# Performance work log

Measured on AMD Instinct MI355X. Metric: run time of the kernel, lower is better.

The kernel has to match this reference:

```python
import jax, jax.numpy as jnp
import numpy as np

LAYERS = 16; SUBLAYERS = 12; NPLANES = LAYERS * SUBLAYERS
POS_LEVEL = 10; DEPTH_LEVEL = 8; ORDER = 3; BASIS_OUT = 8
HIDDEN = 384; BASIS_HIDDEN = 64
SLOPE = 0.01; SIG_OFF = 5.0
IN_H = 512; IN_W = 768; RAYS = 1024
OFFSET = 0.0


def leaky(x):
    return jnp.where(x >= 0, x, SLOPE * x)


def grid_sample_3d(vol, gx, gy, gz):
    # vol (C, D, H, W); grid coords normalized [-1,1]; align_corners=True, zeros padding
    C, Dm, H, W = vol.shape
    x = (gx + 1.0) * 0.5 * (W - 1)
    y = (gy + 1.0) * 0.5 * (H - 1)
    z = (gz + 1.0) * 0.5 * (Dm - 1)
    x0 = jnp.floor(x); y0 = jnp.floor(y); z0 = jnp.floor(z)
    flat = vol.reshape(C, -1)
    out = jnp.zeros((C,) + x.shape, vol.dtype)
    for dz in (0.0, 1.0):
        for dy in (0.0, 1.0):
            for dx in (0.0, 1.0):
                xi = x0 + dx; yi = y0 + dy; zi = z0 + dz
                w = (1 - jnp.abs(x - xi)) * (1 - jnp.abs(y - yi)) * (1 - jnp.abs(z - zi))
                valid = ((xi >= 0) & (xi < W) & (yi >= 0) & (yi < H) & (zi >= 0) & (zi < Dm)).astype(vol.dtype)
                idx = ((jnp.clip(zi, 0, Dm - 1) * H + jnp.clip(yi, 0, H - 1)) * W
                       + jnp.clip(xi, 0, W - 1)).astype(jnp.int32)
                out = out + (w * valid)[None] * jnp.take(flat, idx, axis=1)
    return out


def _rotation(angle, axis):
    axis = np.asarray(axis, np.float64); axis /= np.linalg.norm(axis)
    K = np.array([[0, -axis[2], axis[1]], [axis[2], 0, -axis[0]], [-axis[1], axis[0], 0]])
    R = np.eye(3) + np.sin(angle) * K + (1 - np.cos(angle)) * (K @ K)
    return jnp.asarray(R, jnp.float32)


def setup_inputs() -> dict:
    key = jax.random.key(0)
    ks = jax.random.split(key, 32)
    def lin(i, fan_in, fan_out):
        w = jax.random.normal(ks[i], (fan_in, fan_out), jnp.float32) / np.sqrt(fan_in).astype(np.float32)
        b = jnp.zeros((fan_out,), jnp.float32)
        return w, b
    in_dim = 2 * (2 * POS_LEVEL + DEPTH_LEVEL)     # 56
    out_dim = 1 + BASIS_OUT * 3                    # 25
    w0, b0 = lin(0, in_dim, HIDDEN)
    w1, b1 = lin(1, HIDDEN, HIDDEN)
    w2, b2 = lin(2, HIDDEN, HIDDEN)
    w3, b3 = lin(3, HIDDEN, HIDDEN)
    w4, b4 = lin(4, HIDDEN, HIDDEN)
    wo, bo = lin(5, HIDDEN, out_dim)
    bw0, bb0 = lin(6, 4 * ORDER, BASIS_HIDDEN)
    bw1, bb1 = lin(7, BASIS_HIDDEN, BASIS_HIDDEN)
    bwo, bbo = lin(8, BASIS_HIDDEN, BASIS_OUT)
    mpi_c = jax.random.uniform(ks[20], (LAYERS, 3, IN_H, IN_W), jnp.float32, -1.0, 1.0)
    K = jnp.array([[600.0, 0.0, IN_W / 2.0], [0.0, 600.0, IN_H / 2.0], [0.0, 0.0, 1.0]], jnp.float32)
    planes = jnp.asarray(1.0 / np.linspace(1.0, 0.1, NPLANES), jnp.float32)  # inverse-depth spacing, dmin=1 dmax=10
    selection = jax.random.randint(ks[21], (RAYS,), 0, IN_H * IN_W)
    return dict(
        mpi_c=mpi_c, w0=w0, b0=b0, w1=w1, b1=b1, w2=w2, b2=b2, w3=w3, b3=b3, w4=w4, b4=b4,
        wo=wo, bo=bo, bw0=bw0, bb0=bb0, bw1=bw1, bb1=bb1, bwo=bwo, bbo=bbo,
        ref_rT=jnp.eye(3, dtype=jnp.float32), ref_t=jnp.zeros((3, 1), jnp.float32), ref_k=K,
        feat_r=_rotation(0.03, [0.2, 1.0, 0.1]),
        feat_t=jnp.array([[0.08], [0.03], [0.02]], jnp.float32),
        feat_center=jnp.array([[-0.08], [-0.03], [-0.02]], jnp.float32),
        feat_k=K, planes=planes, selection=selection, out_h=IN_H, out_w=IN_W)


def reference(mpi_c, w0, b0, w1, b1, w2, b2, w3, b3, w4, b4, wo, bo,
              bw0, bb0, bw1, bb1, bwo, bbo,
              ref_rT, ref_t, ref_k, feat_r, feat_t, feat_center, feat_k,
              planes, selection, out_h, out_w):
    # ---- homography warp (computeHomographies / computeHomoWarp) ----
    ki = jnp.linalg.inv(feat_k)
    new_r = feat_r @ ref_rT
    new_t = -new_r @ ref_t + feat_t
    nvec = jnp.array([[0.0, 0.0, 1.0]], jnp.float32)
    Ha = new_r.T
    Hb = Ha @ new_t @ nvec @ Ha
    Hc = (nvec @ Ha @ new_t)[0, 0]
    Hs = ref_k @ (Ha + Hb / (-planes[:, None, None] - Hc)) @ ki      # (P,3,3)
    coords = jnp.stack([(selection % out_w).astype(jnp.float32),
                        (selection // out_w).astype(jnp.float32),
                        jnp.ones_like(selection, jnp.float32)], -1)   # (R,3)
    prod = jnp.einsum('rc,pkc->prk', coords, Hs)                      # (P,R,3)
    ref_coords = prod[..., :2] / prod[..., 2:]                        # (P,R,2)
    scale = jnp.array([IN_W - 1.0, IN_H - 1.0], jnp.float32)
    warp = (ref_coords + OFFSET) / scale * 2.0 - 1.0                  # (P,R,2)
    R = warp.shape[1]

    # ---- positional encoding + main MLP ----
    pos_freq = (0.5 * np.pi) * (2.0 ** jnp.arange(POS_LEVEL, dtype=jnp.float32))
    depth_freq = (0.5 * np.pi) * (2.0 ** jnp.arange(DEPTH_LEVEL, dtype=jnp.float32))
    z_coords = jnp.linspace(-1.0, 1.0, NPLANES)
    vxy = (warp[..., None] * pos_freq).reshape(NPLANES, R, 2 * POS_LEVEL)
    vz = jnp.broadcast_to((z_coords[:, None] * depth_freq[None])[:, None, :], (NPLANES, R, DEPTH_LEVEL))
    vxyz = jnp.concatenate([vxy, vz], -1)
    big = jnp.concatenate([jnp.sin(vxyz), jnp.cos(vxyz)], -1)         # (P,R,56)
    h = leaky(big @ w0 + b0)
    for w_, b_ in ((w1, b1), (w2, b2), (w3, b3), (w4, b4)):
        h = leaky(h @ w_ + b_)
    out = h @ wo + bo                                                 # (P,R,25)
    alpha = jax.nn.sigmoid(out[..., 0] - SIG_OFF)                     # (P,R)

    # ---- trilinear grid sample of sigmoid(mpi_c) ----
    vol = jnp.transpose(jax.nn.sigmoid(mpi_c), (1, 0, 2, 3))          # (3,L,H,W)
    depths = jnp.repeat(jnp.linspace(-1.0, 1.0, LAYERS), SUBLAYERS)   # (P,)
    gz = jnp.broadcast_to(depths[:, None], (NPLANES, R))
    rgb = grid_sample_3d(vol, warp[..., 0], warp[..., 1], gz)         # (3,P,R)
    rgb = jnp.transpose(rgb, (1, 2, 0))                               # (P,R,3)

    # ---- specular basis (viewing-angle MLP) ----
    camera = ref_rT.T @ feat_center + ref_t                           # (3,1)
    coords3 = jnp.concatenate([ref_coords, jnp.ones_like(ref_coords[..., :1])], -1)
    xyz = jnp.einsum('kc,prc->prk', ki, coords3 * planes[:, None, None])
    v = xyz - camera[:, 0]
    v = v / (jnp.linalg.norm(v, axis=-1, keepdims=True) + 1e-7)
    view_freq = 2.0 ** jnp.arange(ORDER, dtype=jnp.float32)
    hv = (v[..., :2, None] * view_freq).reshape(NPLANES, R, 2 * ORDER)
    venc = jnp.concatenate([jnp.sin(0.5 * np.pi * hv), jnp.cos(0.5 * np.pi * hv)], -1)  # (P,R,12)
    bh = leaky(venc @ bw0 + bb0)
    bh = leaky(bh @ bw1 + bb1)
    basis = jnp.tanh(bh @ bwo + bbo)                                  # (P,R,8)
    coeff = jnp.repeat(out[::SUBLAYERS, ..., 1:], SUBLAYERS, axis=0)  # (P,R,24)
    coeff = jnp.tanh(coeff.reshape(NPLANES, R, 3, BASIS_OUT))
    illum = jnp.sum(coeff * basis[:, :, None, :], -1)                 # (P,R,3)
    rgb = jnp.clip(rgb + illum, 0.0, 1.0)

    # ---- alpha compositing (cumprod_exclusive over planes) ----
    cp = jnp.cumprod(1.0 - alpha, axis=0)
    weight = jnp.concatenate([jnp.ones_like(cp[:1]), cp[:-1]], 0)     # (P,R)
    comp = jnp.sum((weight * alpha)[..., None] * rgb, axis=0)         # (R,3)
    return jnp.transpose(comp)[None, :, :, None]                      # (1,3,R,1)
```

## Files before the change

### kernel.cpp

```cpp
#include <hip/hip_runtime.h>
#include <hip/hip_bf16.h>
#include <math.h>


typedef _Float16 half2 __attribute__((ext_vector_type(2)));
typedef _Float16 half4 __attribute__((ext_vector_type(4)));
typedef _Float16 half8 __attribute__((ext_vector_type(8)));
typedef float f32x4 __attribute__((ext_vector_type(4)));

#if __has_builtin(__builtin_amdgcn_mfma_f32_16x16x32_f16)
#define MFMA32(a, b, c) __builtin_amdgcn_mfma_f32_16x16x32_f16((a), (b), (c), 0, 0, 0)
#else
#define MFMA32(a, b, c) (c)
#endif

#define NPLANES 192
#define RAYS    1024
#define IMW     768
#define IMH     512
#define PI_HALF 1.5707964f

#define FR(i, c) ((((i) >> 4) * 6144) + (((c) >> 5) * 512) + ((((c) >> 3) & 3) * 128) \
                  + (((i) & 15) * 8) + ((c) & 7))

__device__ __forceinline__ float sin_rev(float rev) {
  float f, r;
  asm("v_fract_f32 %0, %1" : "=v"(f) : "v"(rev));
  asm("v_sin_f32 %0, %1" : "=v"(r) : "v"(f));
  return r;
}

__device__ __forceinline__ float exp2_fast(float x) {
  float r;
  asm("v_exp_f32 %0, %1" : "=v"(r) : "v"(x));
  return r;
}
__device__ __forceinline__ float rcp_fast(float x) {
  float r;
  asm("v_rcp_f32 %0, %1" : "=v"(r) : "v"(x));
  return r;
}
__device__ __forceinline__ float tanh_fast(float x) {
  const float xc = fminf(fmaxf(x, -30.f), 30.f);
  const float t = exp2_fast(xc * 2.885390082f);
  return (t - 1.f) * rcp_fast(t + 1.f);
}
__device__ __forceinline__ float sig5_fast(float o) {
  const float u = exp2_fast((5.f - o) * 1.4426950f);
  return rcp_fast(1.f + u);
}

__device__ __forceinline__ half4 leaky_pack(f32x4 a) {
  const float v0 = fmaxf(a[0], a[0] * 0.01f);
  const float v1 = fmaxf(a[1], a[1] * 0.01f);
  const float v2 = fmaxf(a[2], a[2] * 0.01f);
  const float v3 = fmaxf(a[3], a[3] * 0.01f);
  const half2 lo = __builtin_bit_cast(half2, __builtin_amdgcn_cvt_pkrtz(v0, v1));
  const half2 hi = __builtin_bit_cast(half2, __builtin_amdgcn_cvt_pkrtz(v2, v3));
  return __builtin_shufflevector(lo, hi, 0, 1, 2, 3);
}

#define O_HS     0
#define O_KICAM  7168
#define O_ALPHA  7424
#define O_COEFF  793856
#define O_PW0    2366720
#define O_PW1    2415872
#define O_PW2    2710784
#define O_PW3    3005696
#define O_PW4    3300608
#define O_PWO    3595520
#define O_PBW0   3620096
#define O_PBW1   3624192
#define O_PBWO   3632384
#define O_BASIS  3634432
#define WS_NEED  (O_BASIS + 6291456)

__global__ void prep_kernel(const float* __restrict__ ref_rT, const float* __restrict__ ref_t,
                            const float* __restrict__ ref_k, const float* __restrict__ feat_r,
                            const float* __restrict__ feat_t, const float* __restrict__ feat_center,
                            const float* __restrict__ feat_k, const float* __restrict__ planes,
                            float* __restrict__ wsHs, float* __restrict__ wsKiCam)
{
  __shared__ float sKi[9], sHa[9], sHb[9], sHc[1];
  if (threadIdx.x == 0) {
    float a = feat_k[0], b = feat_k[1], c = feat_k[2];
    float d = feat_k[3], e = feat_k[4], f = feat_k[5];
    float g = feat_k[6], h = feat_k[7], i = feat_k[8];
    float A = e * i - f * h, B = -(d * i - f * g), C = d * h - e * g;
    float det = a * A + b * B + c * C;
    float id = 1.0f / det;
    float ki[9];
    ki[0] = A * id;             ki[1] = -(b * i - c * h) * id;  ki[2] = (b * f - c * e) * id;
    ki[3] = B * id;             ki[4] = (a * i - c * g) * id;   ki[5] = -(a * f - c * d) * id;
    ki[6] = C * id;             ki[7] = -(a * h - b * g) * id;  ki[8] = (a * e - b * d) * id;
    float nr[9];
    for (int r2 = 0; r2 < 3; ++r2)
      for (int c2 = 0; c2 < 3; ++c2) {
        float s = 0.f;
        for (int k2 = 0; k2 < 3; ++k2) s += feat_r[r2 * 3 + k2] * ref_rT[k2 * 3 + c2];
        nr[r2 * 3 + c2] = s;
      }
    float ntv[3];
    for (int r2 = 0; r2 < 3; ++r2) {
      float s = 0.f;
      for (int k2 = 0; k2 < 3; ++k2) s += nr[r2 * 3 + k2] * ref_t[k2];
      ntv[r2] = -s + feat_t[r2];
    }
    float Ha[9];
    for (int r2 = 0; r2 < 3; ++r2)
      for (int c2 = 0; c2 < 3; ++c2) Ha[r2 * 3 + c2] = nr[c2 * 3 + r2];
    float u[3];
    for (int r2 = 0; r2 < 3; ++r2) {
      float s = 0.f;
      for (int k2 = 0; k2 < 3; ++k2) s += Ha[r2 * 3 + k2] * ntv[k2];
      u[r2] = s;
    }
    float Hb[9];
    for (int r2 = 0; r2 < 3; ++r2)
      for (int c2 = 0; c2 < 3; ++c2) Hb[r2 * 3 + c2] = u[r2] * Ha[6 + c2];
    float cam[3];
    for (int r2 = 0; r2 < 3; ++r2) {
      float s = 0.f;
      for (int k2 = 0; k2 < 3; ++k2) s += ref_rT[k2 * 3 + r2] * feat_center[k2];
      cam[r2] = s + ref_t[r2];
    }
    for (int j = 0; j < 9; ++j) { sKi[j] = ki[j]; sHa[j] = Ha[j]; sHb[j] = Hb[j]; }
    sHc[0] = u[2];
    for (int j = 0; j < 9; ++j) wsKiCam[j] = ki[j];
    for (int j = 0; j < 3; ++j) wsKiCam[9 + j] = cam[j];
  }
  __syncthreads();
  int p = threadIdx.x;
  if (p < NPLANES) {
    float dnm = -planes[p] - sHc[0];
    float T[9];
    for (int j = 0; j < 9; ++j) T[j] = sHa[j] + sHb[j] / dnm;
    float U[9];
    for (int r2 = 0; r2 < 3; ++r2)
      for (int c2 = 0; c2 < 3; ++c2) {
        float s = 0.f;
        for (int k2 = 0; k2 < 3; ++k2) s += ref_k[r2 * 3 + k2] * T[k2 * 3 + c2];
        U[r2 * 3 + c2] = s;
      }
    for (int r2 = 0; r2 < 3; ++r2)
      for (int c2 = 0; c2 < 3; ++c2) {
        float s = 0.f;
        for (int k2 = 0; k2 < 3; ++k2) s += U[r2 * 3 + k2] * sKi[k2 * 3 + c2];
        wsHs[p * 9 + r2 * 3 + c2] = s;
      }
  }
}

__global__ void pack_all_kernel(const float* __restrict__ w0, const float* __restrict__ w1,
                                const float* __restrict__ w2, const float* __restrict__ w3,
                                const float* __restrict__ w4, const float* __restrict__ wo,
                                const float* __restrict__ bw0, const float* __restrict__ bw1,
                                const float* __restrict__ bwo, _Float16* __restrict__ dst)
{
  const int idx = blockIdx.x * 256 + threadIdx.x;
  const float* src; int Ksrc, Nsrc, NP, l;
  if (idx < 24576)       { src = w0;  Ksrc = 56;  Nsrc = 384; NP = 384; l = idx; }
  else if (idx < 172032) { src = w1;  Ksrc = 384; Nsrc = 384; NP = 384; l = idx - 24576; }
  else if (idx < 319488) { src = w2;  Ksrc = 384; Nsrc = 384; NP = 384; l = idx - 172032; }
  else if (idx < 466944) { src = w3;  Ksrc = 384; Nsrc = 384; NP = 384; l = idx - 319488; }
  else if (idx < 614400) { src = w4;  Ksrc = 384; Nsrc = 384; NP = 384; l = idx - 466944; }
  else if (idx < 626688) { src = wo;  Ksrc = 384; Nsrc = 25;  NP = 32;  l = idx - 614400; }
  else if (idx < 628736) { src = bw0; Ksrc = 12;  Nsrc = 64;  NP = 64;  l = idx - 626688; }
  else if (idx < 632832) { src = bw1; Ksrc = 64;  Nsrc = 64;  NP = 64;  l = idx - 628736; }
  else if (idx < 633856) { src = bwo; Ksrc = 64;  Nsrc = 8;   NP = 16;  l = idx - 632832; }
  else return;
  const int within = l & 511, blk = l >> 9;
  const int kg = within >> 7, ln = (within >> 3) & 15, j = within & 7;
  const int ntiles = NP >> 4;
  const int nt = blk % ntiles, kc = blk / ntiles;
  const int k = kc * 32 + kg * 8 + j, nn = nt * 16 + ln;
  const float v = (k < Ksrc && nn < Nsrc) ? src[k * Nsrc + nn] : 0.0f;
  dst[idx] = (_Float16)v;
}

template <int NKC>
__device__ __forceinline__ void hidden_layer(_Float16* hb, const _Float16* __restrict__ wl,
                                             const float* __restrict__ bias,
                                             int wv, int g, int ln, int lane)
{
  f32x4 acc[6][4];
  #pragma unroll
  for (int ft = 0; ft < 6; ++ft) {
    const f32x4 bv4 = *(const f32x4*)&bias[(wv * 6 + ft) * 16 + g * 4];
    #pragma unroll
    for (int pt = 0; pt < 4; ++pt) acc[ft][pt] = bv4;
  }
  #pragma unroll 2
  for (int kc = 0; kc < NKC; ++kc) {
    half8 aw[6];
    #pragma unroll
    for (int ft = 0; ft < 6; ++ft)
      aw[ft] = *(const half8*)&wl[(kc * 24 + wv * 6 + ft) * 512 + lane * 8];
    half8 bx[4];
    #pragma unroll
    for (int pt = 0; pt < 4; ++pt)
      bx[pt] = *(const half8*)&hb[pt * 6144 + kc * 512 + lane * 8];
    #pragma unroll
    for (int ft = 0; ft < 6; ++ft)
      #pragma unroll
      for (int pt = 0; pt < 4; ++pt)
        acc[ft][pt] = MFMA32(aw[ft], bx[pt], acc[ft][pt]);
  }
  __syncthreads();
  #pragma unroll
  for (int pt = 0; pt < 4; ++pt)
    #pragma unroll
    for (int ft = 0; ft < 6; ++ft) {
      const int f0 = wv * 96 + ft * 16 + g * 4;
      *(half4*)&hb[pt * 6144 + (f0 >> 5) * 512 + ((f0 >> 3) & 3) * 128 + ln * 8 + (f0 & 7)] =
          leaky_pack(acc[ft][pt]);
    }
  __syncthreads();
}

template <int NKC>
__device__ __forceinline__ void basis_hidden(_Float16* hb, const _Float16* __restrict__ wl,
                                             const float* __restrict__ bias,
                                             int wv, int g, int ln, int lane)
{
  f32x4 acc[4];
  const f32x4 bv4 = *(const f32x4*)&bias[wv * 16 + g * 4];
  #pragma unroll
  for (int pt = 0; pt < 4; ++pt) acc[pt] = bv4;
  #pragma unroll
  for (int kc = 0; kc < NKC; ++kc) {
    half8 aw = *(const half8*)&wl[(kc * 4 + wv) * 512 + lane * 8];
    #pragma unroll
    for (int pt = 0; pt < 4; ++pt) {
      half8 bx = *(const half8*)&hb[pt * 6144 + kc * 512 + lane * 8];
      acc[pt] = MFMA32(aw, bx, acc[pt]);
    }
  }
  __syncthreads();
  const int f0 = wv * 16 + g * 4;
  #pragma unroll
  for (int pt = 0; pt < 4; ++pt)
    *(half4*)&hb[pt * 6144 + (f0 >> 5) * 512 + ((f0 >> 3) & 3) * 128 + ln * 8 + (f0 & 7)] =
        leaky_pack(acc[pt]);
  __syncthreads();
}

__global__ __launch_bounds__(256, 3) void mlp_kernel(
    const int* __restrict__ selection, const float* __restrict__ planes,
    const float* __restrict__ wsHs, const float* __restrict__ wsKiCam,
    const _Float16* __restrict__ pw0, const _Float16* __restrict__ pw1,
    const _Float16* __restrict__ pw2, const _Float16* __restrict__ pw3,
    const _Float16* __restrict__ pw4, const _Float16* __restrict__ pwo,
    const float* __restrict__ b0, const float* __restrict__ b1,
    const float* __restrict__ b2, const float* __restrict__ b3,
    const float* __restrict__ b4, const float* __restrict__ bo,
    const _Float16* __restrict__ pbw0, const _Float16* __restrict__ pbw1,
    const _Float16* __restrict__ pbwo,
    const float* __restrict__ bb0, const float* __restrict__ bb1,
    const float* __restrict__ bbo,
    float* __restrict__ wsAlpha, float* __restrict__ wsCoeff, float* __restrict__ wsBasis)
{
  __shared__ _Float16 hbuf[4 * 6144];
  const int t = threadIdx.x;
  const int m0 = blockIdx.x * 64;
  const int p = m0 >> 10;
  const int r0 = m0 & 1023;
  const int lane = t & 63, wv = t >> 6;
  const int g = lane >> 4, ln = lane & 15;

  {
    const int i = t >> 2, q = t & 3;
    const int ray = r0 + i;
    const int sel = selection[ray];
    const float cx = (float)(sel % IMW), cy = (float)(sel / IMW);
    const float* H = wsHs + p * 9;
    const float pr0 = H[0] * cx + H[1] * cy + H[2];
    const float pr1 = H[3] * cx + H[4] * cy + H[5];
    const float pr2 = H[6] * cx + H[7] * cy + H[8];
    const float rx = pr0 / pr2, ry = pr1 / pr2;
    const float wx = (rx / 767.0f) * 2.0f - 1.0f;
    const float wy = (ry / 511.0f) * 2.0f - 1.0f;
    const float zc = -1.0f + (float)p * (2.0f / 191.0f);
    #pragma unroll
    for (int cc = 0; cc < 7; ++cc) {
      const int c = q * 7 + cc;
      float base; int e;
      if (c < 10)      { base = wx; e = c; }
      else if (c < 20) { base = wy; e = c - 10; }
      else             { base = zc; e = c - 20; }
      const float rev = ldexpf(base, e - 2);
      hbuf[FR(i, c)]      = (_Float16)sin_rev(rev);
      hbuf[FR(i, c + 28)] = (_Float16)sin_rev(rev + 0.25f);
    }
    hbuf[FR(i, 56 + q)] = (_Float16)0.f;
    hbuf[FR(i, 60 + q)] = (_Float16)0.f;
  }
  __syncthreads();

  hidden_layer<2>(hbuf, pw0, b0, wv, g, ln, lane);
  hidden_layer<12>(hbuf, pw1, b1, wv, g, ln, lane);
  hidden_layer<12>(hbuf, pw2, b2, wv, g, ln, lane);
  hidden_layer<12>(hbuf, pw3, b3, wv, g, ln, lane);
  hidden_layer<12>(hbuf, pw4, b4, wv, g, ln, lane);

  f32x4 acc2[2];
  {
    #pragma unroll
    for (int ft = 0; ft < 2; ++ft) {
      f32x4 bv;
      #pragma unroll
      for (int r = 0; r < 4; ++r) {
        const int f = ft * 16 + g * 4 + r;
        bv[r] = (f < 25) ? bo[f] : 0.f;
      }
      acc2[ft] = bv;
    }
    #pragma unroll 2
    for (int kc = 0; kc < 12; ++kc) {
      half8 bx = *(const half8*)&hbuf[wv * 6144 + kc * 512 + lane * 8];
      #pragma unroll
      for (int ft = 0; ft < 2; ++ft) {
        half8 aw = *(const half8*)&pwo[(kc * 2 + ft) * 512 + lane * 8];
        acc2[ft] = MFMA32(aw, bx, acc2[ft]);
      }
    }
    __syncthreads();
  }

  {
    const int i = t >> 2, q = t & 3;
    const int ray = r0 + i;
    const int sel = selection[ray];
    const float cx = (float)(sel % IMW), cy = (float)(sel / IMW);
    const float* H = wsHs + p * 9;
    const float pr0 = H[0] * cx + H[1] * cy + H[2];
    const float pr1 = H[3] * cx + H[4] * cy + H[5];
    const float pr2 = H[6] * cx + H[7] * cy + H[8];
    const float rx = pr0 / pr2, ry = pr1 / pr2;
    const float pd = planes[p];
    const float* ki = wsKiCam; const float* cam = wsKiCam + 9;
    const float c0 = rx * pd, c1 = ry * pd, c2 = pd;
    const float vx0 = ki[0] * c0 + ki[1] * c1 + ki[2] * c2 - cam[0];
    const float vy0 = ki[3] * c0 + ki[4] * c1 + ki[5] * c2 - cam[1];
    const float vz0 = ki[6] * c0 + ki[7] * c1 + ki[8] * c2 - cam[2];
    const float nrm = sqrtf(vx0 * vx0 + vy0 * vy0 + vz0 * vz0) + 1e-7f;
    const float vx = vx0 / nrm, vy = vy0 / nrm;
    #pragma unroll
    for (int cc = 0; cc < 4; ++cc) {
      const int c = q * 4 + cc;
      float v;
      if (c < 6) {
        v = sin_rev(ldexpf((c < 3) ? vx : vy, (c % 3) - 2));
      } else if (c < 12) {
        const int c6 = c - 6;
        v = sin_rev(ldexpf((c6 < 3) ? vx : vy, (c6 % 3) - 2) + 0.25f);
      } else v = 0.f;
      hbuf[FR(i, c)] = (_Float16)v;
    }
  }
  __syncthreads();

  {
    if (g == 0) {
      const int ray = r0 + wv * 16 + ln;
      wsAlpha[p * RAYS + ray] = sig5_fast(acc2[0][0]);
    }
    if ((p % 12) == 0) {
      const int pg = p / 12;
      const int ray = r0 + wv * 16 + ln;
      #pragma unroll
      for (int ft = 0; ft < 2; ++ft)
        #pragma unroll
        for (int r = 0; r < 4; ++r) {
          const int f = ft * 16 + g * 4 + r;
          if (f >= 1 && f < 25)
            wsCoeff[(pg * 24 + (f - 1)) * RAYS + ray] = tanh_fast(acc2[ft][r]);
        }
    }
  }

  basis_hidden<1>(hbuf, pbw0, bb0, wv, g, ln, lane);
  basis_hidden<2>(hbuf, pbw1, bb1, wv, g, ln, lane);
  {
    f32x4 accO = (f32x4){0.f, 0.f, 0.f, 0.f};
    #pragma unroll
    for (int kc = 0; kc < 2; ++kc) {
      half8 aw = *(const half8*)&pbwo[kc * 512 + lane * 8];
      half8 bx = *(const half8*)&hbuf[wv * 6144 + kc * 512 + lane * 8];
      accO = MFMA32(aw, bx, accO);
    }
    if (g < 2) {
      const int ray = r0 + wv * 16 + ln;
      f32x4 bv;
      #pragma unroll
      for (int r = 0; r < 4; ++r)
        bv[r] = tanh_fast(accO[r] + bbo[g * 4 + r]);
      *(f32x4*)&wsBasis[(p * RAYS + ray) * 8 + g * 4] = bv;
    }
  }
}

__global__ __launch_bounds__(192) void composite_kernel(
    const float* __restrict__ mpi, const int* __restrict__ selection,
    const float* __restrict__ wsHs, const float* __restrict__ wsAlpha,
    const float* __restrict__ wsCoeff, const float* __restrict__ wsBasis,
    float* __restrict__ out)
{
  const int ray = blockIdx.x;
  const int p = threadIdx.x;
  const int sel = selection[ray];
  const float cx = (float)(sel % IMW), cy = (float)(sel / IMW);
  const float* H = wsHs + p * 9;
  const float pr0 = H[0] * cx + H[1] * cy + H[2];
  const float pr1 = H[3] * cx + H[4] * cy + H[5];
  const float pr2 = H[6] * cx + H[7] * cy + H[8];
  const float rx = pr0 / pr2, ry = pr1 / pr2;
  const float wx = (rx / 767.0f) * 2.0f - 1.0f;
  const float wy = (ry / 511.0f) * 2.0f - 1.0f;
  const float x = (wx + 1.0f) * 0.5f * 767.0f;
  const float y = (wy + 1.0f) * 0.5f * 511.0f;
  const float gz = -1.0f + (float)(p / 12) * (2.0f / 15.0f);
  const float z = (gz + 1.0f) * 0.5f * 15.0f;
  const float x0 = floorf(x), y0 = floorf(y), z0 = floorf(z);
  float rgb0 = 0.f, rgb1 = 0.f, rgb2 = 0.f;
  #pragma unroll
  for (int dz = 0; dz < 2; ++dz)
    #pragma unroll
    for (int dy = 0; dy < 2; ++dy)
      #pragma unroll
      for (int dx = 0; dx < 2; ++dx) {
        const float xi = x0 + (float)dx, yi = y0 + (float)dy, zi = z0 + (float)dz;
        const float w = (1.f - fabsf(x - xi)) * (1.f - fabsf(y - yi)) * (1.f - fabsf(z - zi));
        const bool valid = (xi >= 0.f) && (xi < 768.f) && (yi >= 0.f) && (yi < 512.f)
                        && (zi >= 0.f) && (zi < 16.f);
        if (valid && w != 0.f) {
          const int ix = (int)xi, iy = (int)yi, iz = (int)zi;
          const int base = iz * 3 * (IMW * IMH) + iy * IMW + ix;
          const float v0 = mpi[base];
          const float v1 = mpi[base + IMW * IMH];
          const float v2 = mpi[base + 2 * IMW * IMH];
          rgb0 += w * (1.f / (1.f + expf(-v0)));
          rgb1 += w * (1.f / (1.f + expf(-v1)));
          rgb2 += w * (1.f / (1.f + expf(-v2)));
        }
      }
  const float* bs = wsBasis + (p * RAYS + ray) * 8;
  const float* cf = wsCoeff + (p / 12) * 24 * RAYS + ray;
  float il0 = 0.f, il1 = 0.f, il2 = 0.f;
  #pragma unroll
  for (int j = 0; j < 8; ++j) {
    const float bj = bs[j];
    il0 += cf[j * RAYS] * bj;
    il1 += cf[(8 + j) * RAYS] * bj;
    il2 += cf[(16 + j) * RAYS] * bj;
  }
  rgb0 = fminf(fmaxf(rgb0 + il0, 0.f), 1.f);
  rgb1 = fminf(fmaxf(rgb1 + il1, 0.f), 1.f);
  rgb2 = fminf(fmaxf(rgb2 + il2, 0.f), 1.f);
  const float a = wsAlpha[p * RAYS + ray];
  const int lane = p & 63, w64 = p >> 6;
  float xs = 1.f - a;
  #pragma unroll
  for (int off = 1; off < 64; off <<= 1) {
    const float v = __shfl_up(xs, off, 64);
    if (lane >= off) xs *= v;
  }
  __shared__ float wtot[3];
  __shared__ float part[3][3];
  if (lane == 63) wtot[w64] = xs;
  __syncthreads();
  float pre = 1.f;
  #pragma unroll
  for (int q = 0; q < 2; ++q)
    if (q < w64) pre *= wtot[q];
  float excl = __shfl_up(xs, 1, 64);
  if (lane == 0) excl = 1.f;
  const float wa = pre * excl * a;
  float s0 = wa * rgb0, s1 = wa * rgb1, s2 = wa * rgb2;
  #pragma unroll
  for (int off = 32; off >= 1; off >>= 1) {
    s0 += __shfl_down(s0, off, 64);
    s1 += __shfl_down(s1, off, 64);
    s2 += __shfl_down(s2, off, 64);
  }
  if (lane == 0) { part[w64][0] = s0; part[w64][1] = s1; part[w64][2] = s2; }
  __syncthreads();
  if (p == 0) {
    out[0 * RAYS + ray] = part[0][0] + part[1][0] + part[2][0];
    out[1 * RAYS + ray] = part[0][1] + part[1][1] + part[2][1];
    out[2 * RAYS + ray] = part[0][2] + part[1][2] + part[2][2];
  }
}

extern "C" void kernel_launch(void* const* d_in, const int* in_sizes, int n_in,
                              void* d_out, int out_size, void* d_ws, size_t ws_size,
                              hipStream_t stream)
{
  (void)in_sizes; (void)n_in; (void)out_size;
  const float* mpi    = (const float*)d_in[0];
  const float* w0     = (const float*)d_in[1];
  const float* b0     = (const float*)d_in[2];
  const float* w1     = (const float*)d_in[3];
  const float* b1     = (const float*)d_in[4];
  const float* w2     = (const float*)d_in[5];
  const float* b2     = (const float*)d_in[6];
  const float* w3     = (const float*)d_in[7];
  const float* b3     = (const float*)d_in[8];
  const float* w4     = (const float*)d_in[9];
  const float* b4     = (const float*)d_in[10];
  const float* wo     = (const float*)d_in[11];
  const float* bo     = (const float*)d_in[12];
  const float* bw0    = (const float*)d_in[13];
  const float* bb0    = (const float*)d_in[14];
  const float* bw1    = (const float*)d_in[15];
  const float* bb1    = (const float*)d_in[16];
  const float* bwo    = (const float*)d_in[17];
  const float* bbo    = (const float*)d_in[18];
  const float* ref_rT = (const float*)d_in[19];
  const float* ref_t  = (const float*)d_in[20];
  const float* ref_k  = (const float*)d_in[21];
  const float* feat_r = (const float*)d_in[22];
  const float* feat_t = (const float*)d_in[23];
  const float* feat_c = (const float*)d_in[24];
  const float* feat_k = (const float*)d_in[25];
  const float* planes = (const float*)d_in[26];
  const int*   selection = (const int*)d_in[27];
  float* outp = (float*)d_out;
  char* ws = (char*)d_ws;
  if (ws_size < (size_t)WS_NEED) return;

  float* wsHs    = (float*)(ws + O_HS);
  float* wsKiCam = (float*)(ws + O_KICAM);
  float* wsAlpha = (float*)(ws + O_ALPHA);
  float* wsCoeff = (float*)(ws + O_COEFF);
  float* wsBasis = (float*)(ws + O_BASIS);
  _Float16* pw0  = (_Float16*)(ws + O_PW0);
  _Float16* pw1  = (_Float16*)(ws + O_PW1);
  _Float16* pw2  = (_Float16*)(ws + O_PW2);
  _Float16* pw3  = (_Float16*)(ws + O_PW3);
  _Float16* pw4  = (_Float16*)(ws + O_PW4);
  _Float16* pwo  = (_Float16*)(ws + O_PWO);
  _Float16* pbw0 = (_Float16*)(ws + O_PBW0);
  _Float16* pbw1 = (_Float16*)(ws + O_PBW1);
  _Float16* pbwo = (_Float16*)(ws + O_PBWO);

  prep_kernel<<<1, 256, 0, stream>>>(ref_rT, ref_t, ref_k, feat_r, feat_t, feat_c,
                                     feat_k, planes, wsHs, wsKiCam);
  pack_all_kernel<<<2476, 256, 0, stream>>>(w0, w1, w2, w3, w4, wo, bw0, bw1, bwo, pw0);

  mlp_kernel<<<(NPLANES * RAYS) / 64, 256, 0, stream>>>(
      selection, planes, wsHs, wsKiCam,
      pw0, pw1, pw2, pw3, pw4, pwo,
      b0, b1, b2, b3, b4, bo,
      pbw0, pbw1, pbwo, bb0, bb1, bbo,
      wsAlpha, wsCoeff, wsBasis);

  composite_kernel<<<RAYS, NPLANES, 0, stream>>>(mpi, selection, wsHs, wsAlpha,
                                                 wsCoeff, wsBasis, outp);
}
```

Measured before the change: 263.2 us.

## Switch MLP matmuls from 16x16x32 to 32x32x16 MFMA tiles

Rewrites the hidden-layer, output and basis MLP matmuls to use 32x32x16 f16 MFMA instructions instead of 16x16x32. The weight packing and the LDS activation layout are reorganised to match 32-row tiles. Each wave now computes 3x2 tiles of 32x32, which raises arithmetic intensity per operand load and cuts the number of LDS and weight reads. It also brackets the MFMA loops with s_setprio. In exchange, accumulator register use grows, and the output and basis stages leave half the waves idle.

```diff
diff --git a/kernel.cpp b/kernel.cpp
--- a/kernel.cpp
+++ b/kernel.cpp
@@ -7,21 +7,21 @@
 typedef _Float16 half4 __attribute__((ext_vector_type(4)));
 typedef _Float16 half8 __attribute__((ext_vector_type(8)));
 typedef float f32x4 __attribute__((ext_vector_type(4)));
-
-#if __has_builtin(__builtin_amdgcn_mfma_f32_16x16x32_f16)
-#define MFMA32(a, b, c) __builtin_amdgcn_mfma_f32_16x16x32_f16((a), (b), (c), 0, 0, 0)
+typedef float f32x16 __attribute__((ext_vector_type(16)));
+
+#if __has_builtin(__builtin_amdgcn_mfma_f32_32x32x16_f16)
+#define MFMA32x32(a, b, c) __builtin_amdgcn_mfma_f32_32x32x16_f16((a), (b), (c), 0, 0, 0)
 #else
-#define MFMA32(a, b, c) (c)
+#define MFMA32x32(a, b, c) (c)
 #endif
 
 #define NPLANES 192
 #define RAYS    1024
 #define IMW     768
 #define IMH     512
-#define PI_HALF 1.5707964f
-
-#define FR(i, c) ((((i) >> 4) * 6144) + (((c) >> 5) * 512) + ((((c) >> 3) & 3) * 128) \
-                  + (((i) & 15) * 8) + ((c) & 7))
+
+#define FR32(i, c) ((((i) >> 5) * 12288) + (((c) >> 4) * 512) + ((((c) >> 3) & 1) * 256) \
+                    + (((i) & 31) * 8) + ((c) & 7))
 
 __device__ __forceinline__ float sin_rev(float rev) {
   float f, r;
@@ -29,7 +29,6 @@
   asm("v_sin_f32 %0, %1" : "=v"(r) : "v"(f));
   return r;
 }
-
 __device__ __forceinline__ float exp2_fast(float x) {
   float r;
   asm("v_exp_f32 %0, %1" : "=v"(r) : "v"(x));
@@ -50,11 +49,11 @@
   return rcp_fast(1.f + u);
 }
 
-__device__ __forceinline__ half4 leaky_pack(f32x4 a) {
-  const float v0 = fmaxf(a[0], a[0] * 0.01f);
-  const float v1 = fmaxf(a[1], a[1] * 0.01f);
-  const float v2 = fmaxf(a[2], a[2] * 0.01f);
-  const float v3 = fmaxf(a[3], a[3] * 0.01f);
+__device__ __forceinline__ half4 leaky_pack(float a0, float a1, float a2, float a3) {
+  const float v0 = fmaxf(a0, a0 * 0.01f);
+  const float v1 = fmaxf(a1, a1 * 0.01f);
+  const float v2 = fmaxf(a2, a2 * 0.01f);
+  const float v3 = fmaxf(a3, a3 * 0.01f);
   const half2 lo = __builtin_bit_cast(half2, __builtin_amdgcn_cvt_pkrtz(v0, v1));
   const half2 hi = __builtin_bit_cast(half2, __builtin_amdgcn_cvt_pkrtz(v2, v3));
   return __builtin_shufflevector(lo, hi, 0, 1, 2, 3);
@@ -71,8 +70,8 @@
 #define O_PW4    3300608
 #define O_PWO    3595520
 #define O_PBW0   3620096
-#define O_PBW1   3624192
-#define O_PBWO   3632384
+#define O_PBW1   3622144
+#define O_PBWO   3630336
 #define O_BASIS  3634432
 #define WS_NEED  (O_BASIS + 6291456)
 
@@ -159,22 +158,21 @@
                                 const float* __restrict__ bwo, _Float16* __restrict__ dst)
 {
   const int idx = blockIdx.x * 256 + threadIdx.x;
-  const float* src; int Ksrc, Nsrc, NP, l;
-  if (idx < 24576)       { src = w0;  Ksrc = 56;  Nsrc = 384; NP = 384; l = idx; }
-  else if (idx < 172032) { src = w1;  Ksrc = 384; Nsrc = 384; NP = 384; l = idx - 24576; }
-  else if (idx < 319488) { src = w2;  Ksrc = 384; Nsrc = 384; NP = 384; l = idx - 172032; }
-  else if (idx < 466944) { src = w3;  Ksrc = 384; Nsrc = 384; NP = 384; l = idx - 319488; }
-  else if (idx < 614400) { src = w4;  Ksrc = 384; Nsrc = 384; NP = 384; l = idx - 466944; }
-  else if (idx < 626688) { src = wo;  Ksrc = 384; Nsrc = 25;  NP = 32;  l = idx - 614400; }
-  else if (idx < 628736) { src = bw0; Ksrc = 12;  Nsrc = 64;  NP = 64;  l = idx - 626688; }
-  else if (idx < 632832) { src = bw1; Ksrc = 64;  Nsrc = 64;  NP = 64;  l = idx - 628736; }
-  else if (idx < 633856) { src = bwo; Ksrc = 64;  Nsrc = 8;   NP = 16;  l = idx - 632832; }
+  const float* src; int Ksrc, Nsrc, ntiles, l;
+  if (idx < 24576)       { src = w0;  Ksrc = 56;  Nsrc = 384; ntiles = 12; l = idx; }
+  else if (idx < 172032) { src = w1;  Ksrc = 384; Nsrc = 384; ntiles = 12; l = idx - 24576; }
+  else if (idx < 319488) { src = w2;  Ksrc = 384; Nsrc = 384; ntiles = 12; l = idx - 172032; }
+  else if (idx < 466944) { src = w3;  Ksrc = 384; Nsrc = 384; ntiles = 12; l = idx - 319488; }
+  else if (idx < 614400) { src = w4;  Ksrc = 384; Nsrc = 384; ntiles = 12; l = idx - 466944; }
+  else if (idx < 626688) { src = wo;  Ksrc = 384; Nsrc = 25;  ntiles = 1;  l = idx - 614400; }
+  else if (idx < 627712) { src = bw0; Ksrc = 12;  Nsrc = 64;  ntiles = 2;  l = idx - 626688; }
+  else if (idx < 631808) { src = bw1; Ksrc = 64;  Nsrc = 64;  ntiles = 2;  l = idx - 627712; }
+  else if (idx < 633856) { src = bwo; Ksrc = 64;  Nsrc = 8;   ntiles = 1;  l = idx - 631808; }
   else return;
   const int within = l & 511, blk = l >> 9;
-  const int kg = within >> 7, ln = (within >> 3) & 15, j = within & 7;
-  const int ntiles = NP >> 4;
+  const int hi = within >> 8, m = (within >> 3) & 31, j = within & 7;
   const int nt = blk % ntiles, kc = blk / ntiles;
-  const int k = kc * 32 + kg * 8 + j, nn = nt * 16 + ln;
+  const int k = kc * 16 + hi * 8 + j, nn = nt * 32 + m;
   const float v = (k < Ksrc && nn < Nsrc) ? src[k * Nsrc + nn] : 0.0f;
   dst[idx] = (_Float16)v;
 }
@@ -182,39 +180,50 @@
 template <int NKC>
 __device__ __forceinline__ void hidden_layer(_Float16* hb, const _Float16* __restrict__ wl,
                                              const float* __restrict__ bias,
-                                             int wv, int g, int ln, int lane)
-{
-  f32x4 acc[6][4];
-  #pragma unroll
-  for (int ft = 0; ft < 6; ++ft) {
-    const f32x4 bv4 = *(const f32x4*)&bias[(wv * 6 + ft) * 16 + g * 4];
-    #pragma unroll
-    for (int pt = 0; pt < 4; ++pt) acc[ft][pt] = bv4;
-  }
+                                             int wv, int hi, int l31, int lane)
+{
+  f32x16 acc[3][2];
+  #pragma unroll
+  for (int ft = 0; ft < 3; ++ft) {
+    const int ftg = wv * 3 + ft;
+    f32x16 bv;
+    #pragma unroll
+    for (int q = 0; q < 4; ++q) {
+      const f32x4 b4 = *(const f32x4*)&bias[ftg * 32 + q * 8 + hi * 4];
+      bv[q * 4 + 0] = b4[0]; bv[q * 4 + 1] = b4[1];
+      bv[q * 4 + 2] = b4[2]; bv[q * 4 + 3] = b4[3];
+    }
+    acc[ft][0] = bv; acc[ft][1] = bv;
+  }
+  __builtin_amdgcn_s_setprio(1);
   #pragma unroll 2
   for (int kc = 0; kc < NKC; ++kc) {
-    half8 aw[6];
-    #pragma unroll
-    for (int ft = 0; ft < 6; ++ft)
-      aw[ft] = *(const half8*)&wl[(kc * 24 + wv * 6 + ft) * 512 + lane * 8];
-    half8 bx[4];
-    #pragma unroll
-    for (int pt = 0; pt < 4; ++pt)
-      bx[pt] = *(const half8*)&hb[pt * 6144 + kc * 512 + lane * 8];
-    #pragma unroll
-    for (int ft = 0; ft < 6; ++ft)
+    half8 aw[3];
+    #pragma unroll
+    for (int ft = 0; ft < 3; ++ft)
+      aw[ft] = *(const half8*)&wl[(kc * 12 + wv * 3 + ft) * 512 + lane * 8];
+    half8 bx[2];
+    #pragma unroll
+    for (int pt = 0; pt < 2; ++pt)
+      bx[pt] = *(const half8*)&hb[pt * 12288 + kc * 512 + lane * 8];
+    #pragma unroll
+    for (int ft = 0; ft < 3; ++ft)
       #pragma unroll
-      for (int pt = 0; pt < 4; ++pt)
-        acc[ft][pt] = MFMA32(aw[ft], bx[pt], acc[ft][pt]);
-  }
-  __syncthreads();
-  #pragma unroll
-  for (int pt = 0; pt < 4; ++pt)
-    #pragma unroll
-    for (int ft = 0; ft < 6; ++ft) {
-      const int f0 = wv * 96 + ft * 16 + g * 4;
-      *(half4*)&hb[pt * 6144 + (f0 >> 5) * 512 + ((f0 >> 3) & 3) * 128 + ln * 8 + (f0 & 7)] =
-          leaky_pack(acc[ft][pt]);
+      for (int pt = 0; pt < 2; ++pt)
+        acc[ft][pt] = MFMA32x32(aw[ft], bx[pt], acc[ft][pt]);
+  }
+  __builtin_amdgcn_s_setprio(0);
+  __syncthreads();
+  #pragma unroll
+  for (int pt = 0; pt < 2; ++pt)
+    #pragma unroll
+    for (int ft = 0; ft < 3; ++ft) {
+      const int ftg = wv * 3 + ft;
+      #pragma unroll
+      for (int q = 0; q < 4; ++q)
+        *(half4*)&hb[pt * 12288 + (ftg * 2 + (q >> 1)) * 512 + (q & 1) * 256 + l31 * 8 + hi * 4] =
+            leaky_pack(acc[ft][pt][q * 4 + 0], acc[ft][pt][q * 4 + 1],
+                       acc[ft][pt][q * 4 + 2], acc[ft][pt][q * 4 + 3]);
     }
   __syncthreads();
 }
@@ -222,27 +231,29 @@
 template <int NKC>
 __device__ __forceinline__ void basis_hidden(_Float16* hb, const _Float16* __restrict__ wl,
                                              const float* __restrict__ bias,
-                                             int wv, int g, int ln, int lane)
-{
-  f32x4 acc[4];
-  const f32x4 bv4 = *(const f32x4*)&bias[wv * 16 + g * 4];
-  #pragma unroll
-  for (int pt = 0; pt < 4; ++pt) acc[pt] = bv4;
+                                             int wv, int hi, int l31, int lane)
+{
+  const int ft = wv >> 1, pt = wv & 1;
+  f32x16 acc;
+  #pragma unroll
+  for (int q = 0; q < 4; ++q) {
+    const f32x4 b4 = *(const f32x4*)&bias[ft * 32 + q * 8 + hi * 4];
+    acc[q * 4 + 0] = b4[0]; acc[q * 4 + 1] = b4[1];
+    acc[q * 4 + 2] = b4[2]; acc[q * 4 + 3] = b4[3];
+  }
+  __builtin_amdgcn_s_setprio(1);
   #pragma unroll
   for (int kc = 0; kc < NKC; ++kc) {
-    half8 aw = *(const half8*)&wl[(kc * 4 + wv) * 512 + lane * 8];
-    #pragma unroll
-    for (int pt = 0; pt < 4; ++pt) {
-      half8 bx = *(const half8*)&hb[pt * 6144 + kc * 512 + lane * 8];
-      acc[pt] = MFMA32(aw, bx, acc[pt]);
-    }
-  }
-  __syncthreads();
-  const int f0 = wv * 16 + g * 4;
-  #pragma unroll
-  for (int pt = 0; pt < 4; ++pt)
-    *(half4*)&hb[pt * 6144 + (f0 >> 5) * 512 + ((f0 >> 3) & 3) * 128 + ln * 8 + (f0 & 7)] =
-        leaky_pack(acc[pt]);
+    half8 aw = *(const half8*)&wl[(kc * 2 + ft) * 512 + lane * 8];
+    half8 bx = *(const half8*)&hb[pt * 12288 + kc * 512 + lane * 8];
+    acc = MFMA32x32(aw, bx, acc);
+  }
+  __builtin_amdgcn_s_setprio(0);
+  __syncthreads();
+  #pragma unroll
+  for (int q = 0; q < 4; ++q)
+    *(half4*)&hb[pt * 12288 + (ft * 2 + (q >> 1)) * 512 + (q & 1) * 256 + l31 * 8 + hi * 4] =
+        leaky_pack(acc[q * 4 + 0], acc[q * 4 + 1], acc[q * 4 + 2], acc[q * 4 + 3]);
   __syncthreads();
 }
 
@@ -261,13 +272,13 @@
     const float* __restrict__ bbo,
     float* __restrict__ wsAlpha, float* __restrict__ wsCoeff, float* __restrict__ wsBasis)
 {
-  __shared__ _Float16 hbuf[4 * 6144];
+  __shared__ _Float16 hbuf[2 * 12288];
   const int t = threadIdx.x;
   const int m0 = blockIdx.x * 64;
   const int p = m0 >> 10;
   const int r0 = m0 & 1023;
   const int lane = t & 63, wv = t >> 6;
-  const int g = lane >> 4, ln = lane & 15;
+  const int hi = lane >> 5, l31 = lane & 31;
 
   {
     const int i = t >> 2, q = t & 3;
@@ -290,40 +301,36 @@
       else if (c < 20) { base = wy; e = c - 10; }
       else             { base = zc; e = c - 20; }
       const float rev = ldexpf(base, e - 2);
-      hbuf[FR(i, c)]      = (_Float16)sin_rev(rev);
-      hbuf[FR(i, c + 28)] = (_Float16)sin_rev(rev + 0.25f);
-    }
-    hbuf[FR(i, 56 + q)] = (_Float16)0.f;
-    hbuf[FR(i, 60 + q)] = (_Float16)0.f;
-  }
-  __syncthreads();
-
-  hidden_layer<2>(hbuf, pw0, b0, wv, g, ln, lane);
-  hidden_layer<12>(hbuf, pw1, b1, wv, g, ln, lane);
-  hidden_layer<12>(hbuf, pw2, b2, wv, g, ln, lane);
-  hidden_layer<12>(hbuf, pw3, b3, wv, g, ln, lane);
-  hidden_layer<12>(hbuf, pw4, b4, wv, g, ln, lane);
-
-  f32x4 acc2[2];
+      hbuf[FR32(i, c)]      = (_Float16)sin_rev(rev);
+      hbuf[FR32(i, c + 28)] = (_Float16)sin_rev(rev + 0.25f);
+    }
+    hbuf[FR32(i, 56 + q)] = (_Float16)0.f;
+    hbuf[FR32(i, 60 + q)] = (_Float16)0.f;
+  }
+  __syncthreads();
+
+  hidden_layer<4>(hbuf, pw0, b0, wv, hi, l31, lane);
+  hidden_layer<24>(hbuf, pw1, b1, wv, hi, l31, lane);
+  hidden_layer<24>(hbuf, pw2, b2, wv, hi, l31, lane);
+  hidden_layer<24>(hbuf, pw3, b3, wv, hi, l31, lane);
+  hidden_layer<24>(hbuf, pw4, b4, wv, hi, l31, lane);
+
+  f32x16 acc2;
   {
     #pragma unroll
-    for (int ft = 0; ft < 2; ++ft) {
-      f32x4 bv;
-      #pragma unroll
-      for (int r = 0; r < 4; ++r) {
-        const int f = ft * 16 + g * 4 + r;
-        bv[r] = (f < 25) ? bo[f] : 0.f;
+    for (int r = 0; r < 16; ++r) {
+      const int f = (r & 3) + 8 * (r >> 2) + 4 * hi;
+      acc2[r] = (f < 25) ? bo[f] : 0.f;
+    }
+    if (wv < 2) {
+      __builtin_amdgcn_s_setprio(1);
+      #pragma unroll 2
+      for (int kc = 0; kc < 24; ++kc) {
+        half8 bx = *(const half8*)&hbuf[wv * 12288 + kc * 512 + lane * 8];
+        half8 aw = *(const half8*)&pwo[kc * 512 + lane * 8];
+        acc2 = MFMA32x32(aw, bx, acc2);
       }
-      acc2[ft] = bv;
-    }
-    #pragma unroll 2
-    for (int kc = 0; kc < 12; ++kc) {
-      half8 bx = *(const half8*)&hbuf[wv * 6144 + kc * 512 + lane * 8];
-      #pragma unroll
-      for (int ft = 0; ft < 2; ++ft) {
-        half8 aw = *(const half8*)&pwo[(kc * 2 + ft) * 512 + lane * 8];
-        acc2[ft] = MFMA32(aw, bx, acc2[ft]);
-      }
+      __builtin_amdgcn_s_setprio(0);
     }
     __syncthreads();
   }
@@ -356,48 +363,41 @@
         const int c6 = c - 6;
         v = sin_rev(ldexpf((c6 < 3) ? vx : vy, (c6 % 3) - 2) + 0.25f);
       } else v = 0.f;
-      hbuf[FR(i, c)] = (_Float16)v;
-    }
-  }
-  __syncthreads();
-
-  {
-    if (g == 0) {
-      const int ray = r0 + wv * 16 + ln;
-      wsAlpha[p * RAYS + ray] = sig5_fast(acc2[0][0]);
-    }
+      hbuf[FR32(i, c)] = (_Float16)v;
+    }
+  }
+  __syncthreads();
+
+  if (wv < 2) {
+    const int ray = r0 + wv * 32 + l31;
+    if (hi == 0) wsAlpha[p * RAYS + ray] = sig5_fast(acc2[0]);
     if ((p % 12) == 0) {
       const int pg = p / 12;
-      const int ray = r0 + wv * 16 + ln;
       #pragma unroll
-      for (int ft = 0; ft < 2; ++ft)
-        #pragma unroll
-        for (int r = 0; r < 4; ++r) {
-          const int f = ft * 16 + g * 4 + r;
-          if (f >= 1 && f < 25)
-            wsCoeff[(pg * 24 + (f - 1)) * RAYS + ray] = tanh_fast(acc2[ft][r]);
-        }
-    }
-  }
-
-  basis_hidden<1>(hbuf, pbw0, bb0, wv, g, ln, lane);
-  basis_hidden<2>(hbuf, pbw1, bb1, wv, g, ln, lane);
-  {
-    f32x4 accO = (f32x4){0.f, 0.f, 0.f, 0.f};
-    #pragma unroll
-    for (int kc = 0; kc < 2; ++kc) {
+      for (int r = 0; r < 16; ++r) {
+        const int f = (r & 3) + 8 * (r >> 2) + 4 * hi;
+        if (f >= 1 && f < 25)
+          wsCoeff[(pg * 24 + (f - 1)) * RAYS + ray] = tanh_fast(acc2[r]);
+      }
+    }
+  }
+
+  basis_hidden<1>(hbuf, pbw0, bb0, wv, hi, l31, lane);
+  basis_hidden<4>(hbuf, pbw1, bb1, wv, hi, l31, lane);
+  if (wv < 2) {
+    f32x16 accO = {};
+    #pragma unroll
+    for (int kc = 0; kc < 4; ++kc) {
       half8 aw = *(const half8*)&pbwo[kc * 512 + lane * 8];
-      half8 bx = *(const half8*)&hbuf[wv * 6144 + kc * 512 + lane * 8];
-      accO = MFMA32(aw, bx, accO);
-    }
-    if (g < 2) {
-      const int ray = r0 + wv * 16 + ln;
-      f32x4 bv;
-      #pragma unroll
-      for (int r = 0; r < 4; ++r)
-        bv[r] = tanh_fast(accO[r] + bbo[g * 4 + r]);
-      *(f32x4*)&wsBasis[(p * RAYS + ray) * 8 + g * 4] = bv;
-    }
+      half8 bx = *(const half8*)&hbuf[wv * 12288 + kc * 512 + lane * 8];
+      accO = MFMA32x32(aw, bx, accO);
+    }
+    const int ray = r0 + wv * 32 + l31;
+    f32x4 bv;
+    #pragma unroll
+    for (int s = 0; s < 4; ++s)
+      bv[s] = tanh_fast(accO[s] + bbo[hi * 4 + s]);
+    *(f32x4*)&wsBasis[(p * RAYS + ray) * 8 + hi * 4] = bv;
   }
 }
 
```

Result: slower. 297.5 us (+13.0%).

## Prefetch next layer weights, hoist view encoding, ping-pong basis MLP buffers

Applied to the files above, without the earlier changes.

Before each layer's barrier, the first K-chunk of the next hidden layer's weights is loaded into registers, so that chunk's global-memory latency overlaps the current layer's epilogue. The view-direction encoding is now computed next to the positional encoding, which removes a second recomputation of the homography, and the values are held in registers until they are written. The basis MLP layers write into separate regions of shared memory, which removes one barrier per basis layer. The cost is more live registers (24 extra VGPRs for the prefetched weights plus 4 for the encoding), which could pressure occupancy under launch_bounds(256,3).

```diff
diff --git a/kernel.cpp b/kernel.cpp
--- a/kernel.cpp
+++ b/kernel.cpp
@@ -18,7 +18,6 @@
 #define RAYS    1024
 #define IMW     768
 #define IMH     512
-#define PI_HALF 1.5707964f
 
 #define FR(i, c) ((((i) >> 4) * 6144) + (((c) >> 5) * 512) + ((((c) >> 3) & 3) * 128) \
                   + (((i) & 15) * 8) + ((c) & 7))
@@ -29,7 +28,6 @@
   asm("v_sin_f32 %0, %1" : "=v"(r) : "v"(f));
   return r;
 }
-
 __device__ __forceinline__ float exp2_fast(float x) {
   float r;
   asm("v_exp_f32 %0, %1" : "=v"(r) : "v"(x));
@@ -179,9 +177,17 @@
   dst[idx] = (_Float16)v;
 }
 
-template <int NKC>
+__device__ __forceinline__ void pre6(half8 awp[6], const _Float16* __restrict__ w,
+                                     int wv, int lane) {
+  #pragma unroll
+  for (int ft = 0; ft < 6; ++ft)
+    awp[ft] = *(const half8*)&w[(wv * 6 + ft) * 512 + lane * 8];
+}
+
+template <int NKC, bool PRE>
 __device__ __forceinline__ void hidden_layer(_Float16* hb, const _Float16* __restrict__ wl,
-                                             const float* __restrict__ bias,
+                                             const _Float16* __restrict__ wlnext,
+                                             const float* __restrict__ bias, half8 awp[6],
                                              int wv, int g, int ln, int lane)
 {
   f32x4 acc[6][4];
@@ -191,8 +197,19 @@
     #pragma unroll
     for (int pt = 0; pt < 4; ++pt) acc[ft][pt] = bv4;
   }
+  {
+    half8 bx[4];
+    #pragma unroll
+    for (int pt = 0; pt < 4; ++pt)
+      bx[pt] = *(const half8*)&hb[pt * 6144 + lane * 8];
+    #pragma unroll
+    for (int ft = 0; ft < 6; ++ft)
+      #pragma unroll
+      for (int pt = 0; pt < 4; ++pt)
+        acc[ft][pt] = MFMA32(awp[ft], bx[pt], acc[ft][pt]);
+  }
   #pragma unroll 2
-  for (int kc = 0; kc < NKC; ++kc) {
+  for (int kc = 1; kc < NKC; ++kc) {
     half8 aw[6];
     #pragma unroll
     for (int ft = 0; ft < 6; ++ft)
@@ -207,6 +224,7 @@
       for (int pt = 0; pt < 4; ++pt)
         acc[ft][pt] = MFMA32(aw[ft], bx[pt], acc[ft][pt]);
   }
+  if (PRE) pre6(awp, wlnext, wv, lane);
   __syncthreads();
   #pragma unroll
   for (int pt = 0; pt < 4; ++pt)
@@ -222,6 +240,7 @@
 template <int NKC>
 __device__ __forceinline__ void basis_hidden(_Float16* hb, const _Float16* __restrict__ wl,
                                              const float* __restrict__ bias,
+                                             int src_kc, int dstC,
                                              int wv, int g, int ln, int lane)
 {
   f32x4 acc[4];
@@ -233,17 +252,15 @@
     half8 aw = *(const half8*)&wl[(kc * 4 + wv) * 512 + lane * 8];
     #pragma unroll
     for (int pt = 0; pt < 4; ++pt) {
-      half8 bx = *(const half8*)&hb[pt * 6144 + kc * 512 + lane * 8];
+      half8 bx = *(const half8*)&hb[pt * 6144 + (src_kc + kc) * 512 + lane * 8];
       acc[pt] = MFMA32(aw, bx, acc[pt]);
     }
   }
-  __syncthreads();
-  const int f0 = wv * 16 + g * 4;
+  const int f0 = dstC + wv * 16 + g * 4;
   #pragma unroll
   for (int pt = 0; pt < 4; ++pt)
     *(half4*)&hb[pt * 6144 + (f0 >> 5) * 512 + ((f0 >> 3) & 3) * 128 + ln * 8 + (f0 & 7)] =
         leaky_pack(acc[pt]);
-  __syncthreads();
 }
 
 __global__ __launch_bounds__(256, 3) void mlp_kernel(
@@ -269,6 +286,10 @@
   const int lane = t & 63, wv = t >> 6;
   const int g = lane >> 4, ln = lane & 15;
 
+  half8 awp[6];
+  pre6(awp, pw0, wv, lane);
+
+  float vencv[4];
   {
     const int i = t >> 2, q = t & 3;
     const int ray = r0 + i;
@@ -295,49 +316,7 @@
     }
     hbuf[FR(i, 56 + q)] = (_Float16)0.f;
     hbuf[FR(i, 60 + q)] = (_Float16)0.f;
-  }
-  __syncthreads();
-
-  hidden_layer<2>(hbuf, pw0, b0, wv, g, ln, lane);
-  hidden_layer<12>(hbuf, pw1, b1, wv, g, ln, lane);
-  hidden_layer<12>(hbuf, pw2, b2, wv, g, ln, lane);
-  hidden_layer<12>(hbuf, pw3, b3, wv, g, ln, lane);
-  hidden_layer<12>(hbuf, pw4, b4, wv, g, ln, lane);
-
-  f32x4 acc2[2];
-  {
-    #pragma unroll
-    for (int ft = 0; ft < 2; ++ft) {
-      f32x4 bv;
-      #pragma unroll
-      for (int r = 0; r < 4; ++r) {
-        const int f = ft * 16 + g * 4 + r;
-        bv[r] = (f < 25) ? bo[f] : 0.f;
-      }
-      acc2[ft] = bv;
-    }
-    #pragma unroll 2
-    for (int kc = 0; kc < 12; ++kc) {
-      half8 bx = *(const half8*)&hbuf[wv * 6144 + kc * 512 + lane * 8];
-      #pragma unroll
-      for (int ft = 0; ft < 2; ++ft) {
-        half8 aw = *(const half8*)&pwo[(kc * 2 + ft) * 512 + lane * 8];
-        acc2[ft] = MFMA32(aw, bx, acc2[ft]);
-      }
-    }
-    __syncthreads();
-  }
-
-  {
-    const int i = t >> 2, q = t & 3;
-    const int ray = r0 + i;
-    const int sel = selection[ray];
-    const float cx = (float)(sel % IMW), cy = (float)(sel / IMW);
-    const float* H = wsHs + p * 9;
-    const float pr0 = H[0] * cx + H[1] * cy + H[2];
-    const float pr1 = H[3] * cx + H[4] * cy + H[5];
-    const float pr2 = H[6] * cx + H[7] * cy + H[8];
-    const float rx = pr0 / pr2, ry = pr1 / pr2;
+
     const float pd = planes[p];
     const float* ki = wsKiCam; const float* cam = wsKiCam + 9;
     const float c0 = rx * pd, c1 = ry * pd, c2 = pd;
@@ -356,8 +335,46 @@
         const int c6 = c - 6;
         v = sin_rev(ldexpf((c6 < 3) ? vx : vy, (c6 % 3) - 2) + 0.25f);
       } else v = 0.f;
-      hbuf[FR(i, c)] = (_Float16)v;
-    }
+      vencv[cc] = v;
+    }
+  }
+  __syncthreads();
+
+  hidden_layer<2,  true >(hbuf, pw0, pw1, b0, awp, wv, g, ln, lane);
+  hidden_layer<12, true >(hbuf, pw1, pw2, b1, awp, wv, g, ln, lane);
+  hidden_layer<12, true >(hbuf, pw2, pw3, b2, awp, wv, g, ln, lane);
+  hidden_layer<12, true >(hbuf, pw3, pw4, b3, awp, wv, g, ln, lane);
+  hidden_layer<12, false>(hbuf, pw4, pw4, b4, awp, wv, g, ln, lane);
+
+  f32x4 acc2[2];
+  {
+    #pragma unroll
+    for (int ft = 0; ft < 2; ++ft) {
+      f32x4 bv;
+      #pragma unroll
+      for (int r = 0; r < 4; ++r) {
+        const int f = ft * 16 + g * 4 + r;
+        bv[r] = (f < 25) ? bo[f] : 0.f;
+      }
+      acc2[ft] = bv;
+    }
+    #pragma unroll 2
+    for (int kc = 0; kc < 12; ++kc) {
+      half8 bx = *(const half8*)&hbuf[wv * 6144 + kc * 512 + lane * 8];
+      #pragma unroll
+      for (int ft = 0; ft < 2; ++ft) {
+        half8 aw = *(const half8*)&pwo[(kc * 2 + ft) * 512 + lane * 8];
+        acc2[ft] = MFMA32(aw, bx, acc2[ft]);
+      }
+    }
+    __syncthreads();
+  }
+
+  {
+    const int i = t >> 2, q = t & 3;
+    #pragma unroll
+    for (int cc = 0; cc < 4; ++cc)
+      hbuf[FR(i, q * 4 + cc)] = (_Float16)vencv[cc];
   }
   __syncthreads();
 
@@ -380,14 +397,16 @@
     }
   }
 
-  basis_hidden<1>(hbuf, pbw0, bb0, wv, g, ln, lane);
-  basis_hidden<2>(hbuf, pbw1, bb1, wv, g, ln, lane);
+  basis_hidden<1>(hbuf, pbw0, bb0, 0, 64, wv, g, ln, lane);
+  __syncthreads();
+  basis_hidden<2>(hbuf, pbw1, bb1, 2, 128, wv, g, ln, lane);
+  __syncthreads();
   {
     f32x4 accO = (f32x4){0.f, 0.f, 0.f, 0.f};
     #pragma unroll
     for (int kc = 0; kc < 2; ++kc) {
       half8 aw = *(const half8*)&pbwo[kc * 512 + lane * 8];
-      half8 bx = *(const half8*)&hbuf[wv * 6144 + kc * 512 + lane * 8];
+      half8 bx = *(const half8*)&hbuf[wv * 6144 + (4 + kc) * 512 + lane * 8];
       accO = MFMA32(aw, bx, accO);
     }
     if (g < 2) {
```

Measured after the change: 409.4 us. 1.56x slower.
